# Kernel optimization log

Measured on AMD Instinct MI355X. Metric: run time of the kernel, lower is better.

Reference implementation:

```python
import jax, jax.numpy as jnp
import numpy as np

N = 1 << 20          # query points
RES = 160            # ceil((xyz_max - xyz_min)/voxel_size) = ceil(1/0.00625)
C = 12               # feature_dim
W = 128              # MLP width
NF = 2               # n_frame_features
FREQS = np.asarray([1.0, 2.0, 4.0, 8.0], np.float32)  # 2**linspace(0,3,4)
DIM0 = C + (3 + 2 * 3 * len(FREQS)) + NF              # 12 + 27 + 2 = 41
XYZ_MIN = np.zeros(3, np.float32)
XYZ_MAX = np.ones(3, np.float32)


def _lin_init(key, fan_in, fan_out):
    kw, kb = jax.random.split(key)
    s = 1.0 / np.sqrt(fan_in)
    w = jax.random.uniform(kw, (fan_in, fan_out), jnp.float32, -s, s)
    b = jax.random.uniform(kb, (fan_out,), jnp.float32, -s, s)
    return w, b


def setup_inputs() -> dict:
    key = jax.random.key(0)
    ks = jax.random.split(key, 10)
    pts = jax.random.uniform(ks[0], (N, 3), jnp.float32)          # inside [xyz_min, xyz_max]
    ff = jax.random.normal(ks[1], (N, NF), jnp.float32)           # frame features
    vd = jax.random.normal(ks[2], (N, 3), jnp.float32)            # view dirs
    vd = vd / jnp.linalg.norm(vd, axis=-1, keepdims=True)
    x = jnp.concatenate([pts, ff, vd], axis=-1)                   # [N, 8]
    grid = jax.random.normal(ks[3], (RES, RES, RES, C), jnp.float32) * 0.1
    dW1, db1 = _lin_init(ks[4], C, W)
    dW2, db2 = _lin_init(ks[5], W, W)
    dW3, _ = _lin_init(ks[6], W, 1)
    db3 = jnp.zeros((1,), jnp.float32)                            # constant bias init 0
    rW1, rb1 = _lin_init(ks[7], DIM0, W)
    rW2, rb2 = _lin_init(ks[8], W, W)
    rW3, _ = _lin_init(ks[9], W, 3)
    rb3 = jnp.zeros((3,), jnp.float32)
    return {"x": x, "grid": grid,
            "dW1": dW1, "db1": db1, "dW2": dW2, "db2": db2, "dW3": dW3, "db3": db3,
            "rW1": rW1, "rb1": rb1, "rW2": rW2, "rb2": rb2, "rW3": rW3, "rb3": rb3}


def trilinear(grid, pts):
    # DenseGrid: grid_sample(mode='bilinear', align_corners=True) on [C, Nx, Ny, Nz]
    R = grid.shape[0]
    u = jnp.clip((pts - XYZ_MIN) / (XYZ_MAX - XYZ_MIN), 0.0, 1.0)  # [N,3] in [0,1]
    pos = u * (R - 1)
    i0 = jnp.clip(jnp.floor(pos), 0, R - 2).astype(jnp.int32)      # [N,3]
    w = pos - i0.astype(pos.dtype)                                 # [N,3]
    g = grid.reshape(-1, grid.shape[-1])                           # [R^3, C]
    x0, y0, z0 = i0[:, 0], i0[:, 1], i0[:, 2]
    x1, y1, z1 = x0 + 1, y0 + 1, z0 + 1
    wx, wy, wz = w[:, 0:1], w[:, 1:2], w[:, 2:3]

    def gat(ix, iy, iz):
        return g[(ix * R + iy) * R + iz]                           # [N, C]

    return ((gat(x0, y0, z0) * (1 - wz) + gat(x0, y0, z1) * wz) * (1 - wy) +
            (gat(x0, y1, z0) * (1 - wz) + gat(x0, y1, z1) * wz) * wy) * (1 - wx) + \
           ((gat(x1, y0, z0) * (1 - wz) + gat(x1, y0, z1) * wz) * (1 - wy) +
            (gat(x1, y1, z0) * (1 - wz) + gat(x1, y1, z1) * wz) * wy) * wx


def view_embed(v):
    # include_input + sin/cos at freqs 2^[0..3]
    parts = [v]
    for f in FREQS:
        parts.append(jnp.sin(v * f))
        parts.append(jnp.cos(v * f))
    return jnp.concatenate(parts, axis=-1)  # [N, 27]


def reference(x, grid, dW1, db1, dW2, db2, dW3, db3, rW1, rb1, rW2, rb2, rW3, rb3):
    pts, ff, vd = x[:, :3], x[:, 3:3 + NF], x[:, 3 + NF:]
    feature = trilinear(grid, pts)                                  # [N, 12]
    h = jax.nn.relu(feature @ dW1 + db1)
    h = jax.nn.relu(h @ dW2 + db2)
    sdf = h @ dW3 + db3                                             # [N, 1]
    rgb_feat = jnp.concatenate([feature, view_embed(vd), ff], -1)  # [N, 41]
    h = jax.nn.relu(rgb_feat @ rW1 + rb1)
    h = jax.nn.relu(h @ rW2 + rb2)
    rgb = h @ rW3 + rb3                                             # [N, 3]
    return jnp.concatenate([rgb, sdf], -1)                          # [N, 4]
```

## Files before the change

### kernel.cpp

```cpp
#include <hip/hip_runtime.h>


#define NPTS   (1 << 20)
#define NCHUNK (NPTS / 64)

typedef _Float16 half8  __attribute__((ext_vector_type(8)));
typedef _Float16 half4_t __attribute__((ext_vector_type(4)));
typedef float    f32x4  __attribute__((ext_vector_type(4)));

#define OFF_DW1T 0
#define OFF_DW2T 4096
#define OFF_RW1A 20480
#define OFF_RW1B 24576
#define OFF_RW2T 28672
#define HALFS_TOTAL 45056
#define OFF_RW3T_BYTES (HALFS_TOTAL * 2)

#define HSTR 136
#define FSTR 40

__global__ void prep_weights(const float* __restrict__ dW1,
                             const float* __restrict__ dW2,
                             const float* __restrict__ rW1,
                             const float* __restrict__ rW2,
                             const float* __restrict__ rW3,
                             _Float16* __restrict__ wsh,
                             float* __restrict__ rw3t)
{
    int tid = blockIdx.x * 256 + threadIdx.x;
    if (tid >= 16384) return;
    int n = tid >> 7, k = tid & 127;
    wsh[OFF_DW2T + n*128 + k] = (_Float16)dW2[k*128 + n];
    wsh[OFF_RW2T + n*128 + k] = (_Float16)rW2[k*128 + n];
    if (k < 32) {
        wsh[OFF_DW1T + n*32 + k] = (k < 12) ? (_Float16)dW1[k*128 + n] : (_Float16)0.f;
        wsh[OFF_RW1A + n*32 + k] = (k < 12) ? (_Float16)rW1[k*128 + n] : (_Float16)0.f;
        wsh[OFF_RW1B + n*32 + k] = (k < 29) ? (_Float16)rW1[(12 + k)*128 + n] : (_Float16)0.f;
    }
    if (k < 3) rw3t[k*128 + n] = rW3[n*3 + k];
}

__device__ __forceinline__ void store_act(_Float16* buf, int n, int ub,
                                          f32x4 acc, const float* __restrict__ bias)
{
    float4 b4 = *(const float4*)(bias + ub);
    half4_t v;
    v[0] = (_Float16)fmaxf(acc[0] + b4.x, 0.f);
    v[1] = (_Float16)fmaxf(acc[1] + b4.y, 0.f);
    v[2] = (_Float16)fmaxf(acc[2] + b4.z, 0.f);
    v[3] = (_Float16)fmaxf(acc[3] + b4.w, 0.f);
    *(half4_t*)(buf + n*HSTR + ub) = v;
}

#define MFMA(a, b, c) __builtin_amdgcn_mfma_f32_16x16x32_f16((a), (b), (c), 0, 0, 0)

__global__ __launch_bounds__(256) void fastsurf_main(
    const float* __restrict__ x, const float* __restrict__ grid,
    const float* __restrict__ db1, const float* __restrict__ db2,
    const float* __restrict__ dW3, const float* __restrict__ db3,
    const float* __restrict__ rb1, const float* __restrict__ rb2,
    const float* __restrict__ rb3,
    const _Float16* __restrict__ wsh, const float* __restrict__ rw3t,
    float* __restrict__ out)
{
    __shared__ _Float16 featA[64 * FSTR];
    __shared__ _Float16 embA [64 * FSTR];
    __shared__ _Float16 h1buf[64 * HSTR];
    __shared__ _Float16 h2buf[64 * HSTR];

    const int t  = threadIdx.x;
    const int wv = t >> 6;
    const int l  = t & 63;
    const int ln = l & 15;
    const int qd = l >> 4;
    const int p  = t >> 2;
    const int q  = t & 3;
    const int u0 = (wv*2 + 0) * 16;
    const int u1 = (wv*2 + 1) * 16;

    half8 a_d2[2][4], a_r2[2][4];
#pragma unroll
    for (int rt = 0; rt < 2; ++rt) {
        const int m = (wv*2 + rt)*16 + ln;
#pragma unroll
        for (int ks = 0; ks < 4; ++ks) {
            a_d2[rt][ks] = *(const half8*)(wsh + OFF_DW2T + m*128 + ks*32 + qd*8);
            a_r2[rt][ks] = *(const half8*)(wsh + OFF_RW2T + m*128 + ks*32 + qd*8);
        }
    }

    for (int chunk = blockIdx.x; chunk < NCHUNK; chunk += gridDim.x) {
        const int pbase = chunk * 64;

        {
            const int P = pbase + p;
            const float4 xa = *(const float4*)(x + (size_t)P*8);
            const float4 xb = *(const float4*)(x + (size_t)P*8 + 4);
            float ux = fminf(fmaxf(xa.x, 0.f), 1.f) * 159.f;
            float uy = fminf(fmaxf(xa.y, 0.f), 1.f) * 159.f;
            float uz = fminf(fmaxf(xa.z, 0.f), 1.f) * 159.f;
            float fx = fminf(floorf(ux), 158.f);
            float fy = fminf(floorf(uy), 158.f);
            float fz = fminf(floorf(uz), 158.f);
            int ix = (int)fx, iy = (int)fy, iz = (int)fz;
            float wx = ux - fx, wy = uy - fy, wz = uz - fz;

            const int bx = q >> 1, by = q & 1;
            float wxy = (bx ? wx : 1.f - wx) * (by ? wy : 1.f - wy);
            float s0 = wxy * (1.f - wz), s1 = wxy * wz;
            const float* c = grid + (size_t)(((ix + bx)*160 + (iy + by))*160 + iz) * 12;
            float4 A0 = *(const float4*)(c);
            float4 A1 = *(const float4*)(c + 4);
            float4 A2 = *(const float4*)(c + 8);
            float4 B0 = *(const float4*)(c + 12);
            float4 B1 = *(const float4*)(c + 16);
            float4 B2 = *(const float4*)(c + 20);
            float f[12];
            f[0] = s0*A0.x + s1*B0.x;  f[1] = s0*A0.y + s1*B0.y;
            f[2] = s0*A0.z + s1*B0.z;  f[3] = s0*A0.w + s1*B0.w;
            f[4] = s0*A1.x + s1*B1.x;  f[5] = s0*A1.y + s1*B1.y;
            f[6] = s0*A1.z + s1*B1.z;  f[7] = s0*A1.w + s1*B1.w;
            f[8] = s0*A2.x + s1*B2.x;  f[9] = s0*A2.y + s1*B2.y;
            f[10]= s0*A2.z + s1*B2.z;  f[11]= s0*A2.w + s1*B2.w;
#pragma unroll
            for (int j = 0; j < 12; ++j) {
                f[j] += __shfl_xor(f[j], 1);
                f[j] += __shfl_xor(f[j], 2);
            }
            half8 fv = { (_Float16)0.f,(_Float16)0.f,(_Float16)0.f,(_Float16)0.f,
                         (_Float16)0.f,(_Float16)0.f,(_Float16)0.f,(_Float16)0.f };
            if (q == 0) {
                fv[0]=(_Float16)f[0]; fv[1]=(_Float16)f[1]; fv[2]=(_Float16)f[2]; fv[3]=(_Float16)f[3];
                fv[4]=(_Float16)f[4]; fv[5]=(_Float16)f[5]; fv[6]=(_Float16)f[6]; fv[7]=(_Float16)f[7];
            } else if (q == 1) {
                fv[0]=(_Float16)f[8]; fv[1]=(_Float16)f[9]; fv[2]=(_Float16)f[10]; fv[3]=(_Float16)f[11];
            }
            *(half8*)(featA + p*FSTR + q*8) = fv;

            const float v0 = xb.y, v1 = xb.z, v2 = xb.w;
            const float ff0 = xa.w, ff1 = xb.x;
            half8 ev = { (_Float16)0.f,(_Float16)0.f,(_Float16)0.f,(_Float16)0.f,
                         (_Float16)0.f,(_Float16)0.f,(_Float16)0.f,(_Float16)0.f };
            if (q == 0) {
                ev[0]=(_Float16)v0; ev[1]=(_Float16)v1; ev[2]=(_Float16)v2;
                ev[3]=(_Float16)__sinf(v0); ev[4]=(_Float16)__sinf(v1); ev[5]=(_Float16)__sinf(v2);
                ev[6]=(_Float16)__cosf(v0); ev[7]=(_Float16)__cosf(v1);
            } else if (q == 1) {
                ev[0]=(_Float16)__cosf(v2);
                ev[1]=(_Float16)__sinf(2.f*v0); ev[2]=(_Float16)__sinf(2.f*v1); ev[3]=(_Float16)__sinf(2.f*v2);
                ev[4]=(_Float16)__cosf(2.f*v0); ev[5]=(_Float16)__cosf(2.f*v1); ev[6]=(_Float16)__cosf(2.f*v2);
                ev[7]=(_Float16)__sinf(4.f*v0);
            } else if (q == 2) {
                ev[0]=(_Float16)__sinf(4.f*v1); ev[1]=(_Float16)__sinf(4.f*v2);
                ev[2]=(_Float16)__cosf(4.f*v0); ev[3]=(_Float16)__cosf(4.f*v1); ev[4]=(_Float16)__cosf(4.f*v2);
                ev[5]=(_Float16)__sinf(8.f*v0); ev[6]=(_Float16)__sinf(8.f*v1); ev[7]=(_Float16)__sinf(8.f*v2);
            } else {
                ev[0]=(_Float16)__cosf(8.f*v0); ev[1]=(_Float16)__cosf(8.f*v1); ev[2]=(_Float16)__cosf(8.f*v2);
                ev[3]=(_Float16)ff0; ev[4]=(_Float16)ff1;
            }
            *(half8*)(embA + p*FSTR + q*8) = ev;
        }
        __syncthreads();

        {
            const half8 a0 = *(const half8*)(wsh + OFF_DW1T + (u0 + ln)*32 + qd*8);
            const half8 a1 = *(const half8*)(wsh + OFF_DW1T + (u1 + ln)*32 + qd*8);
#pragma unroll
            for (int tl = 0; tl < 4; ++tl) {
                const int n = tl*16 + ln;
                half8 b = *(const half8*)(featA + n*FSTR + qd*8);
                f32x4 z = {0.f, 0.f, 0.f, 0.f};
                f32x4 acc0 = MFMA(a0, b, z);
                f32x4 acc1 = MFMA(a1, b, z);
                store_act(h1buf, n, u0 + qd*4, acc0, db1);
                store_act(h1buf, n, u1 + qd*4, acc1, db1);
            }
        }
        __syncthreads();

        {
#pragma unroll
            for (int tl = 0; tl < 4; ++tl) {
                const int n = tl*16 + ln;
                f32x4 acc0 = {0.f,0.f,0.f,0.f}, acc1 = {0.f,0.f,0.f,0.f};
#pragma unroll
                for (int ks = 0; ks < 4; ++ks) {
                    half8 b = *(const half8*)(h1buf + n*HSTR + ks*32 + qd*8);
                    acc0 = MFMA(a_d2[0][ks], b, acc0);
                    acc1 = MFMA(a_d2[1][ks], b, acc1);
                }
                store_act(h2buf, n, u0 + qd*4, acc0, db2);
                store_act(h2buf, n, u1 + qd*4, acc1, db2);
            }
        }
        __syncthreads();

        float sdf;
        {
            float s = 0.f;
#pragma unroll
            for (int i = 0; i < 4; ++i) {
                const int kb = q*32 + i*8;
                half8 hv = *(const half8*)(h2buf + p*HSTR + kb);
                float4 wa = *(const float4*)(dW3 + kb);
                float4 wb = *(const float4*)(dW3 + kb + 4);
                s += (float)hv[0]*wa.x + (float)hv[1]*wa.y + (float)hv[2]*wa.z + (float)hv[3]*wa.w
                   + (float)hv[4]*wb.x + (float)hv[5]*wb.y + (float)hv[6]*wb.z + (float)hv[7]*wb.w;
            }
            s += __shfl_xor(s, 1);
            s += __shfl_xor(s, 2);
            sdf = s + db3[0];
        }

        {
            const half8 aa0 = *(const half8*)(wsh + OFF_RW1A + (u0 + ln)*32 + qd*8);
            const half8 aa1 = *(const half8*)(wsh + OFF_RW1A + (u1 + ln)*32 + qd*8);
            const half8 ab0 = *(const half8*)(wsh + OFF_RW1B + (u0 + ln)*32 + qd*8);
            const half8 ab1 = *(const half8*)(wsh + OFF_RW1B + (u1 + ln)*32 + qd*8);
#pragma unroll
            for (int tl = 0; tl < 4; ++tl) {
                const int n = tl*16 + ln;
                half8 bf = *(const half8*)(featA + n*FSTR + qd*8);
                half8 be = *(const half8*)(embA  + n*FSTR + qd*8);
                f32x4 acc0 = {0.f,0.f,0.f,0.f}, acc1 = {0.f,0.f,0.f,0.f};
                acc0 = MFMA(aa0, bf, acc0);  acc0 = MFMA(ab0, be, acc0);
                acc1 = MFMA(aa1, bf, acc1);  acc1 = MFMA(ab1, be, acc1);
                store_act(h1buf, n, u0 + qd*4, acc0, rb1);
                store_act(h1buf, n, u1 + qd*4, acc1, rb1);
            }
        }
        __syncthreads();

        {
#pragma unroll
            for (int tl = 0; tl < 4; ++tl) {
                const int n = tl*16 + ln;
                f32x4 acc0 = {0.f,0.f,0.f,0.f}, acc1 = {0.f,0.f,0.f,0.f};
#pragma unroll
                for (int ks = 0; ks < 4; ++ks) {
                    half8 b = *(const half8*)(h1buf + n*HSTR + ks*32 + qd*8);
                    acc0 = MFMA(a_r2[0][ks], b, acc0);
                    acc1 = MFMA(a_r2[1][ks], b, acc1);
                }
                store_act(h2buf, n, u0 + qd*4, acc0, rb2);
                store_act(h2buf, n, u1 + qd*4, acc1, rb2);
            }
        }
        __syncthreads();

        {
            float r0 = 0.f, r1 = 0.f, r2 = 0.f;
#pragma unroll
            for (int i = 0; i < 4; ++i) {
                const int kb = q*32 + i*8;
                half8 hv = *(const half8*)(h2buf + p*HSTR + kb);
                float h0=hv[0], h1v=hv[1], h2v=hv[2], h3=hv[3], h4=hv[4], h5=hv[5], h6=hv[6], h7=hv[7];
                {
                    float4 wa = *(const float4*)(rw3t + kb);
                    float4 wb = *(const float4*)(rw3t + kb + 4);
                    r0 += h0*wa.x + h1v*wa.y + h2v*wa.z + h3*wa.w + h4*wb.x + h5*wb.y + h6*wb.z + h7*wb.w;
                }
                {
                    float4 wa = *(const float4*)(rw3t + 128 + kb);
                    float4 wb = *(const float4*)(rw3t + 128 + kb + 4);
                    r1 += h0*wa.x + h1v*wa.y + h2v*wa.z + h3*wa.w + h4*wb.x + h5*wb.y + h6*wb.z + h7*wb.w;
                }
                {
                    float4 wa = *(const float4*)(rw3t + 256 + kb);
                    float4 wb = *(const float4*)(rw3t + 256 + kb + 4);
                    r2 += h0*wa.x + h1v*wa.y + h2v*wa.z + h3*wa.w + h4*wb.x + h5*wb.y + h6*wb.z + h7*wb.w;
                }
            }
            r0 += __shfl_xor(r0, 1);  r0 += __shfl_xor(r0, 2);
            r1 += __shfl_xor(r1, 1);  r1 += __shfl_xor(r1, 2);
            r2 += __shfl_xor(r2, 1);  r2 += __shfl_xor(r2, 2);
            if (q == 0) {
                float4 o;
                o.x = r0 + rb3[0];
                o.y = r1 + rb3[1];
                o.z = r2 + rb3[2];
                o.w = sdf;
                *(float4*)(out + (size_t)(pbase + p)*4) = o;
            }
        }
        __syncthreads();
    }
}

extern "C" void kernel_launch(void* const* d_in, const int* in_sizes, int n_in,
                              void* d_out, int out_size, void* d_ws, size_t ws_size,
                              hipStream_t stream) {
    const float* x    = (const float*)d_in[0];
    const float* grid = (const float*)d_in[1];
    const float* dW1  = (const float*)d_in[2];
    const float* db1  = (const float*)d_in[3];
    const float* dW2  = (const float*)d_in[4];
    const float* db2  = (const float*)d_in[5];
    const float* dW3  = (const float*)d_in[6];
    const float* db3  = (const float*)d_in[7];
    const float* rW1  = (const float*)d_in[8];
    const float* rb1  = (const float*)d_in[9];
    const float* rW2  = (const float*)d_in[10];
    const float* rb2  = (const float*)d_in[11];
    const float* rW3  = (const float*)d_in[12];
    const float* rb3  = (const float*)d_in[13];
    float* out = (float*)d_out;

    _Float16* wsh = (_Float16*)d_ws;
    float* rw3t = (float*)((char*)d_ws + OFF_RW3T_BYTES);

    prep_weights<<<64, 256, 0, stream>>>(dW1, dW2, rW1, rW2, rW3, wsh, rw3t);
    fastsurf_main<<<1024, 256, 0, stream>>>(x, grid, db1, db2, dW3, db3,
                                            rb1, rb2, rb3, wsh, rw3t, out);
}
```

Measured before the change: 668.2 us.

## Prefetch next chunk's gathers and merge density/RGB MLP stages to cut barriers

The input points and trilinear corner gathers for the next chunk are software-prefetched into registers while the current chunk's MLPs run. A barrier that waits only on LDS counters lets those global loads stay in flight across synchronisation points. The density and RGB MLP layers are merged stage by stage into separate LDS buffers, which cuts the per-chunk barriers from six to three. The cost is roughly double the shared memory plus extra prefetch registers, which may reduce occupancy.

Measured after the change: 767.0 us. 14.8% more time.

```diff
diff --git a/kernel.cpp b/kernel.cpp
--- a/kernel.cpp
+++ b/kernel.cpp
@@ -54,6 +54,29 @@
 
 #define MFMA(a, b, c) __builtin_amdgcn_mfma_f32_16x16x32_f16((a), (b), (c), 0, 0, 0)
 
+__device__ __forceinline__ void wg_barrier() {
+    asm volatile("s_waitcnt lgkmcnt(0)" ::: "memory");
+    __builtin_amdgcn_s_barrier();
+}
+
+__device__ __forceinline__ const float* corner_addr(const float* __restrict__ grid,
+                                                    float4 xa, int bx, int by,
+                                                    float& s0, float& s1)
+{
+    float ux = fminf(fmaxf(xa.x, 0.f), 1.f) * 159.f;
+    float uy = fminf(fmaxf(xa.y, 0.f), 1.f) * 159.f;
+    float uz = fminf(fmaxf(xa.z, 0.f), 1.f) * 159.f;
+    float fx = fminf(floorf(ux), 158.f);
+    float fy = fminf(floorf(uy), 158.f);
+    float fz = fminf(floorf(uz), 158.f);
+    int ix = (int)fx, iy = (int)fy, iz = (int)fz;
+    float wx = ux - fx, wy = uy - fy, wz = uz - fz;
+    float wxy = (bx ? wx : 1.f - wx) * (by ? wy : 1.f - wy);
+    s0 = wxy * (1.f - wz);
+    s1 = wxy * wz;
+    return grid + (size_t)(((ix + bx)*160 + (iy + by))*160 + iz) * 12;
+}
+
 __global__ __launch_bounds__(256) void fastsurf_main(
     const float* __restrict__ x, const float* __restrict__ grid,
     const float* __restrict__ db1, const float* __restrict__ db2,
@@ -67,6 +90,8 @@
     __shared__ _Float16 embA [64 * FSTR];
     __shared__ _Float16 h1buf[64 * HSTR];
     __shared__ _Float16 h2buf[64 * HSTR];
+    __shared__ _Float16 g1buf[64 * HSTR];
+    __shared__ _Float16 g2buf[64 * HSTR];
 
     const int t  = threadIdx.x;
     const int wv = t >> 6;
@@ -75,8 +100,10 @@
     const int qd = l >> 4;
     const int p  = t >> 2;
     const int q  = t & 3;
+    const int bx = q >> 1, by = q & 1;
     const int u0 = (wv*2 + 0) * 16;
     const int u1 = (wv*2 + 1) * 16;
+    const int STEP = gridDim.x;
 
     half8 a_d2[2][4], a_r2[2][4];
 #pragma unroll
@@ -89,39 +116,37 @@
         }
     }
 
-    for (int chunk = blockIdx.x; chunk < NCHUNK; chunk += gridDim.x) {
+    float4 xc_a, xc_b;
+    float4 xn_a, xn_b;
+    float  s0c, s1c;
+    float4 gA0, gA1, gA2, gB0, gB1, gB2;
+
+    {
+        int c0 = blockIdx.x;
+        int c1 = c0 + STEP; if (c1 >= NCHUNK) c1 = c0;
+        size_t P0 = (size_t)c0*64 + p;
+        xc_a = *(const float4*)(x + P0*8);
+        xc_b = *(const float4*)(x + P0*8 + 4);
+        size_t P1 = (size_t)c1*64 + p;
+        xn_a = *(const float4*)(x + P1*8);
+        xn_b = *(const float4*)(x + P1*8 + 4);
+        const float* cb = corner_addr(grid, xc_a, bx, by, s0c, s1c);
+        gA0 = *(const float4*)(cb);      gA1 = *(const float4*)(cb + 4);
+        gA2 = *(const float4*)(cb + 8);  gB0 = *(const float4*)(cb + 12);
+        gB1 = *(const float4*)(cb + 16); gB2 = *(const float4*)(cb + 20);
+    }
+
+    for (int chunk = blockIdx.x; chunk < NCHUNK; chunk += STEP) {
         const int pbase = chunk * 64;
 
         {
-            const int P = pbase + p;
-            const float4 xa = *(const float4*)(x + (size_t)P*8);
-            const float4 xb = *(const float4*)(x + (size_t)P*8 + 4);
-            float ux = fminf(fmaxf(xa.x, 0.f), 1.f) * 159.f;
-            float uy = fminf(fmaxf(xa.y, 0.f), 1.f) * 159.f;
-            float uz = fminf(fmaxf(xa.z, 0.f), 1.f) * 159.f;
-            float fx = fminf(floorf(ux), 158.f);
-            float fy = fminf(floorf(uy), 158.f);
-            float fz = fminf(floorf(uz), 158.f);
-            int ix = (int)fx, iy = (int)fy, iz = (int)fz;
-            float wx = ux - fx, wy = uy - fy, wz = uz - fz;
-
-            const int bx = q >> 1, by = q & 1;
-            float wxy = (bx ? wx : 1.f - wx) * (by ? wy : 1.f - wy);
-            float s0 = wxy * (1.f - wz), s1 = wxy * wz;
-            const float* c = grid + (size_t)(((ix + bx)*160 + (iy + by))*160 + iz) * 12;
-            float4 A0 = *(const float4*)(c);
-            float4 A1 = *(const float4*)(c + 4);
-            float4 A2 = *(const float4*)(c + 8);
-            float4 B0 = *(const float4*)(c + 12);
-            float4 B1 = *(const float4*)(c + 16);
-            float4 B2 = *(const float4*)(c + 20);
             float f[12];
-            f[0] = s0*A0.x + s1*B0.x;  f[1] = s0*A0.y + s1*B0.y;
-            f[2] = s0*A0.z + s1*B0.z;  f[3] = s0*A0.w + s1*B0.w;
-            f[4] = s0*A1.x + s1*B1.x;  f[5] = s0*A1.y + s1*B1.y;
-            f[6] = s0*A1.z + s1*B1.z;  f[7] = s0*A1.w + s1*B1.w;
-            f[8] = s0*A2.x + s1*B2.x;  f[9] = s0*A2.y + s1*B2.y;
-            f[10]= s0*A2.z + s1*B2.z;  f[11]= s0*A2.w + s1*B2.w;
+            f[0] = s0c*gA0.x + s1c*gB0.x;  f[1] = s0c*gA0.y + s1c*gB0.y;
+            f[2] = s0c*gA0.z + s1c*gB0.z;  f[3] = s0c*gA0.w + s1c*gB0.w;
+            f[4] = s0c*gA1.x + s1c*gB1.x;  f[5] = s0c*gA1.y + s1c*gB1.y;
+            f[6] = s0c*gA1.z + s1c*gB1.z;  f[7] = s0c*gA1.w + s1c*gB1.w;
+            f[8] = s0c*gA2.x + s1c*gB2.x;  f[9] = s0c*gA2.y + s1c*gB2.y;
+            f[10]= s0c*gA2.z + s1c*gB2.z;  f[11]= s0c*gA2.w + s1c*gB2.w;
 #pragma unroll
             for (int j = 0; j < 12; ++j) {
                 f[j] += __shfl_xor(f[j], 1);
@@ -137,8 +162,8 @@
             }
             *(half8*)(featA + p*FSTR + q*8) = fv;
 
-            const float v0 = xb.y, v1 = xb.z, v2 = xb.w;
-            const float ff0 = xa.w, ff1 = xb.x;
+            const float v0 = xc_b.y, v1 = xc_b.z, v2 = xc_b.w;
+            const float ff0 = xc_a.w, ff1 = xc_b.x;
             half8 ev = { (_Float16)0.f,(_Float16)0.f,(_Float16)0.f,(_Float16)0.f,
                          (_Float16)0.f,(_Float16)0.f,(_Float16)0.f,(_Float16)0.f };
             if (q == 0) {
@@ -160,23 +185,46 @@
             }
             *(half8*)(embA + p*FSTR + q*8) = ev;
         }
-        __syncthreads();
-
-        {
-            const half8 a0 = *(const half8*)(wsh + OFF_DW1T + (u0 + ln)*32 + qd*8);
-            const half8 a1 = *(const half8*)(wsh + OFF_DW1T + (u1 + ln)*32 + qd*8);
+
+        {
+            float s0n, s1n;
+            const float* cb = corner_addr(grid, xn_a, bx, by, s0n, s1n);
+            xc_a = xn_a; xc_b = xn_b;
+            s0c = s0n;  s1c = s1n;
+            gA0 = *(const float4*)(cb);      gA1 = *(const float4*)(cb + 4);
+            gA2 = *(const float4*)(cb + 8);  gB0 = *(const float4*)(cb + 12);
+            gB1 = *(const float4*)(cb + 16); gB2 = *(const float4*)(cb + 20);
+            int c2 = chunk + 2*STEP; if (c2 >= NCHUNK) c2 = chunk;
+            size_t P2 = (size_t)c2*64 + p;
+            xn_a = *(const float4*)(x + P2*8);
+            xn_b = *(const float4*)(x + P2*8 + 4);
+        }
+        wg_barrier();
+
+        {
+            const half8 ad0 = *(const half8*)(wsh + OFF_DW1T + (u0 + ln)*32 + qd*8);
+            const half8 ad1 = *(const half8*)(wsh + OFF_DW1T + (u1 + ln)*32 + qd*8);
+            const half8 aa0 = *(const half8*)(wsh + OFF_RW1A + (u0 + ln)*32 + qd*8);
+            const half8 aa1 = *(const half8*)(wsh + OFF_RW1A + (u1 + ln)*32 + qd*8);
+            const half8 ab0 = *(const half8*)(wsh + OFF_RW1B + (u0 + ln)*32 + qd*8);
+            const half8 ab1 = *(const half8*)(wsh + OFF_RW1B + (u1 + ln)*32 + qd*8);
 #pragma unroll
             for (int tl = 0; tl < 4; ++tl) {
                 const int n = tl*16 + ln;
-                half8 b = *(const half8*)(featA + n*FSTR + qd*8);
+                half8 bf = *(const half8*)(featA + n*FSTR + qd*8);
+                half8 be = *(const half8*)(embA  + n*FSTR + qd*8);
                 f32x4 z = {0.f, 0.f, 0.f, 0.f};
-                f32x4 acc0 = MFMA(a0, b, z);
-                f32x4 acc1 = MFMA(a1, b, z);
-                store_act(h1buf, n, u0 + qd*4, acc0, db1);
-                store_act(h1buf, n, u1 + qd*4, acc1, db1);
-            }
-        }
-        __syncthreads();
+                f32x4 d0 = MFMA(ad0, bf, z);
+                f32x4 d1 = MFMA(ad1, bf, z);
+                store_act(h1buf, n, u0 + qd*4, d0, db1);
+                store_act(h1buf, n, u1 + qd*4, d1, db1);
+                f32x4 r0 = MFMA(aa0, bf, z);  r0 = MFMA(ab0, be, r0);
+                f32x4 r1 = MFMA(aa1, bf, z);  r1 = MFMA(ab1, be, r1);
+                store_act(g1buf, n, u0 + qd*4, r0, rb1);
+                store_act(g1buf, n, u1 + qd*4, r1, rb1);
+            }
+        }
+        wg_barrier();
 
         {
 #pragma unroll
@@ -191,70 +239,33 @@
                 }
                 store_act(h2buf, n, u0 + qd*4, acc0, db2);
                 store_act(h2buf, n, u1 + qd*4, acc1, db2);
-            }
-        }
-        __syncthreads();
-
-        float sdf;
-        {
-            float s = 0.f;
+                f32x4 rcc0 = {0.f,0.f,0.f,0.f}, rcc1 = {0.f,0.f,0.f,0.f};
+#pragma unroll
+                for (int ks = 0; ks < 4; ++ks) {
+                    half8 b = *(const half8*)(g1buf + n*HSTR + ks*32 + qd*8);
+                    rcc0 = MFMA(a_r2[0][ks], b, rcc0);
+                    rcc1 = MFMA(a_r2[1][ks], b, rcc1);
+                }
+                store_act(g2buf, n, u0 + qd*4, rcc0, rb2);
+                store_act(g2buf, n, u1 + qd*4, rcc1, rb2);
+            }
+        }
+        wg_barrier();
+
+        {
+            float sacc = 0.f, r0 = 0.f, r1 = 0.f, r2 = 0.f;
 #pragma unroll
             for (int i = 0; i < 4; ++i) {
                 const int kb = q*32 + i*8;
                 half8 hv = *(const half8*)(h2buf + p*HSTR + kb);
-                float4 wa = *(const float4*)(dW3 + kb);
-                float4 wb = *(const float4*)(dW3 + kb + 4);
-                s += (float)hv[0]*wa.x + (float)hv[1]*wa.y + (float)hv[2]*wa.z + (float)hv[3]*wa.w
-                   + (float)hv[4]*wb.x + (float)hv[5]*wb.y + (float)hv[6]*wb.z + (float)hv[7]*wb.w;
-            }
-            s += __shfl_xor(s, 1);
-            s += __shfl_xor(s, 2);
-            sdf = s + db3[0];
-        }
-
-        {
-            const half8 aa0 = *(const half8*)(wsh + OFF_RW1A + (u0 + ln)*32 + qd*8);
-            const half8 aa1 = *(const half8*)(wsh + OFF_RW1A + (u1 + ln)*32 + qd*8);
-            const half8 ab0 = *(const half8*)(wsh + OFF_RW1B + (u0 + ln)*32 + qd*8);
-            const half8 ab1 = *(const half8*)(wsh + OFF_RW1B + (u1 + ln)*32 + qd*8);
-#pragma unroll
-            for (int tl = 0; tl < 4; ++tl) {
-                const int n = tl*16 + ln;
-                half8 bf = *(const half8*)(featA + n*FSTR + qd*8);
-                half8 be = *(const half8*)(embA  + n*FSTR + qd*8);
-                f32x4 acc0 = {0.f,0.f,0.f,0.f}, acc1 = {0.f,0.f,0.f,0.f};
-                acc0 = MFMA(aa0, bf, acc0);  acc0 = MFMA(ab0, be, acc0);
-                acc1 = MFMA(aa1, bf, acc1);  acc1 = MFMA(ab1, be, acc1);
-                store_act(h1buf, n, u0 + qd*4, acc0, rb1);
-                store_act(h1buf, n, u1 + qd*4, acc1, rb1);
-            }
-        }
-        __syncthreads();
-
-        {
-#pragma unroll
-            for (int tl = 0; tl < 4; ++tl) {
-                const int n = tl*16 + ln;
-                f32x4 acc0 = {0.f,0.f,0.f,0.f}, acc1 = {0.f,0.f,0.f,0.f};
-#pragma unroll
-                for (int ks = 0; ks < 4; ++ks) {
-                    half8 b = *(const half8*)(h1buf + n*HSTR + ks*32 + qd*8);
-                    acc0 = MFMA(a_r2[0][ks], b, acc0);
-                    acc1 = MFMA(a_r2[1][ks], b, acc1);
-                }
-                store_act(h2buf, n, u0 + qd*4, acc0, rb2);
-                store_act(h2buf, n, u1 + qd*4, acc1, rb2);
-            }
-        }
-        __syncthreads();
-
-        {
-            float r0 = 0.f, r1 = 0.f, r2 = 0.f;
-#pragma unroll
-            for (int i = 0; i < 4; ++i) {
-                const int kb = q*32 + i*8;
-                half8 hv = *(const half8*)(h2buf + p*HSTR + kb);
-                float h0=hv[0], h1v=hv[1], h2v=hv[2], h3=hv[3], h4=hv[4], h5=hv[5], h6=hv[6], h7=hv[7];
+                {
+                    float4 wa = *(const float4*)(dW3 + kb);
+                    float4 wb = *(const float4*)(dW3 + kb + 4);
+                    sacc += (float)hv[0]*wa.x + (float)hv[1]*wa.y + (float)hv[2]*wa.z + (float)hv[3]*wa.w
+                          + (float)hv[4]*wb.x + (float)hv[5]*wb.y + (float)hv[6]*wb.z + (float)hv[7]*wb.w;
+                }
+                half8 gv = *(const half8*)(g2buf + p*HSTR + kb);
+                float h0=gv[0], h1v=gv[1], h2v=gv[2], h3=gv[3], h4=gv[4], h5=gv[5], h6=gv[6], h7=gv[7];
                 {
                     float4 wa = *(const float4*)(rw3t + kb);
                     float4 wb = *(const float4*)(rw3t + kb + 4);
@@ -271,6 +282,7 @@
                     r2 += h0*wa.x + h1v*wa.y + h2v*wa.z + h3*wa.w + h4*wb.x + h5*wb.y + h6*wb.z + h7*wb.w;
                 }
             }
+            sacc += __shfl_xor(sacc, 1);  sacc += __shfl_xor(sacc, 2);
             r0 += __shfl_xor(r0, 1);  r0 += __shfl_xor(r0, 2);
             r1 += __shfl_xor(r1, 1);  r1 += __shfl_xor(r1, 2);
             r2 += __shfl_xor(r2, 1);  r2 += __shfl_xor(r2, 2);
@@ -279,11 +291,10 @@
                 o.x = r0 + rb3[0];
                 o.y = r1 + rb3[1];
                 o.z = r2 + rb3[2];
-                o.w = sdf;
+                o.w = sacc + db3[0];
                 *(float4*)(out + (size_t)(pbase + p)*4) = o;
             }
         }
-        __syncthreads();
     }
 }
 
```

## Swizzle LDS activations, run output layers on MFMA, reload layer-2 weights per chunk

Applied to the files above, without the earlier changes.

Replaces the padded LDS strides with an XOR-swizzled layout for the feature/embedding and hidden buffers, merging the feature and embedding buffers into one. The final sdf and rgb projections now use MFMA with fp16 weights prepared in workspace, replacing the scalar dot products and shuffle reductions. Layer-2 weight fragments are loaded from global/L2 inside each chunk instead of being held in registers across the loop, and launch bounds request 4 blocks per CU. This cuts register pressure and LDS bank conflicts, at the cost of repeated weight loads and fp16 rounding of the output weights.

Result: slower. 784.4 us (+17.4%).

```diff
diff --git a/kernel.cpp b/kernel.cpp
--- a/kernel.cpp
+++ b/kernel.cpp
@@ -4,28 +4,26 @@
 #define NPTS   (1 << 20)
 #define NCHUNK (NPTS / 64)
 
-typedef _Float16 half8  __attribute__((ext_vector_type(8)));
+typedef _Float16 half8   __attribute__((ext_vector_type(8)));
 typedef _Float16 half4_t __attribute__((ext_vector_type(4)));
-typedef float    f32x4  __attribute__((ext_vector_type(4)));
+typedef float    f32x4   __attribute__((ext_vector_type(4)));
 
 #define OFF_DW1T 0
 #define OFF_DW2T 4096
 #define OFF_RW1A 20480
 #define OFF_RW1B 24576
 #define OFF_RW2T 28672
-#define HALFS_TOTAL 45056
-#define OFF_RW3T_BYTES (HALFS_TOTAL * 2)
-
-#define HSTR 136
-#define FSTR 40
+#define OFF_RGBA 45056
+#define OFF_SDFA 45568
+#define HALFS_TOTAL 45696
 
 __global__ void prep_weights(const float* __restrict__ dW1,
                              const float* __restrict__ dW2,
+                             const float* __restrict__ dW3,
                              const float* __restrict__ rW1,
                              const float* __restrict__ rW2,
                              const float* __restrict__ rW3,
-                             _Float16* __restrict__ wsh,
-                             float* __restrict__ rw3t)
+                             _Float16* __restrict__ wsh)
 {
     int tid = blockIdx.x * 256 + threadIdx.x;
     if (tid >= 16384) return;
@@ -37,7 +35,8 @@
         wsh[OFF_RW1A + n*32 + k] = (k < 12) ? (_Float16)rW1[k*128 + n] : (_Float16)0.f;
         wsh[OFF_RW1B + n*32 + k] = (k < 29) ? (_Float16)rW1[(12 + k)*128 + n] : (_Float16)0.f;
     }
-    if (k < 3) rw3t[k*128 + n] = rW3[n*3 + k];
+    if (n < 4)  wsh[OFF_RGBA + n*128 + k] = (n < 3) ? (_Float16)rW3[k*3 + n] : (_Float16)0.f;
+    if (n == 0) wsh[OFF_SDFA + k] = (_Float16)dW3[k];
 }
 
 __device__ __forceinline__ void store_act(_Float16* buf, int n, int ub,
@@ -49,24 +48,27 @@
     v[1] = (_Float16)fmaxf(acc[1] + b4.y, 0.f);
     v[2] = (_Float16)fmaxf(acc[2] + b4.z, 0.f);
     v[3] = (_Float16)fmaxf(acc[3] + b4.w, 0.f);
-    *(half4_t*)(buf + n*HSTR + ub) = v;
+    const int u = ub >> 3;
+    *(half4_t*)(buf + n*128 + ((u ^ (n & 7)) << 3) + (ub & 7)) = v;
 }
 
 #define MFMA(a, b, c) __builtin_amdgcn_mfma_f32_16x16x32_f16((a), (b), (c), 0, 0, 0)
 
-__global__ __launch_bounds__(256) void fastsurf_main(
+#define HRD(buf, n, ks, qd) (*(const half8*)((buf) + (n)*128 + ((((ks)*4 + (qd)) ^ ((n) & 7)) << 3)))
+#define FRD(n, u) (*(const half8*)(fe + (n)*64 + (((u) ^ ((n) & 7)) << 3)))
+
+__global__ __launch_bounds__(256, 4) void fastsurf_main(
     const float* __restrict__ x, const float* __restrict__ grid,
     const float* __restrict__ db1, const float* __restrict__ db2,
-    const float* __restrict__ dW3, const float* __restrict__ db3,
+    const float* __restrict__ db3,
     const float* __restrict__ rb1, const float* __restrict__ rb2,
     const float* __restrict__ rb3,
-    const _Float16* __restrict__ wsh, const float* __restrict__ rw3t,
+    const _Float16* __restrict__ wsh,
     float* __restrict__ out)
 {
-    __shared__ _Float16 featA[64 * FSTR];
-    __shared__ _Float16 embA [64 * FSTR];
-    __shared__ _Float16 h1buf[64 * HSTR];
-    __shared__ _Float16 h2buf[64 * HSTR];
+    __shared__ _Float16 fe[64 * 64];
+    __shared__ _Float16 h1[64 * 128];
+    __shared__ _Float16 h2[64 * 128];
 
     const int t  = threadIdx.x;
     const int wv = t >> 6;
@@ -78,16 +80,8 @@
     const int u0 = (wv*2 + 0) * 16;
     const int u1 = (wv*2 + 1) * 16;
 
-    half8 a_d2[2][4], a_r2[2][4];
-#pragma unroll
-    for (int rt = 0; rt < 2; ++rt) {
-        const int m = (wv*2 + rt)*16 + ln;
-#pragma unroll
-        for (int ks = 0; ks < 4; ++ks) {
-            a_d2[rt][ks] = *(const half8*)(wsh + OFF_DW2T + m*128 + ks*32 + qd*8);
-            a_r2[rt][ks] = *(const half8*)(wsh + OFF_RW2T + m*128 + ks*32 + qd*8);
-        }
-    }
+    const float db3v = db3[0];
+    const float rb30 = rb3[0], rb31 = rb3[1], rb32 = rb3[2];
 
     for (int chunk = blockIdx.x; chunk < NCHUNK; chunk += gridDim.x) {
         const int pbase = chunk * 64;
@@ -135,7 +129,7 @@
             } else if (q == 1) {
                 fv[0]=(_Float16)f[8]; fv[1]=(_Float16)f[9]; fv[2]=(_Float16)f[10]; fv[3]=(_Float16)f[11];
             }
-            *(half8*)(featA + p*FSTR + q*8) = fv;
+            *(half8*)(fe + p*64 + ((q ^ (p & 7)) << 3)) = fv;
 
             const float v0 = xb.y, v1 = xb.z, v2 = xb.w;
             const float ff0 = xa.w, ff1 = xb.x;
@@ -158,7 +152,7 @@
                 ev[0]=(_Float16)__cosf(8.f*v0); ev[1]=(_Float16)__cosf(8.f*v1); ev[2]=(_Float16)__cosf(8.f*v2);
                 ev[3]=(_Float16)ff0; ev[4]=(_Float16)ff1;
             }
-            *(half8*)(embA + p*FSTR + q*8) = ev;
+            *(half8*)(fe + p*64 + (((4 + q) ^ (p & 7)) << 3)) = ev;
         }
         __syncthreads();
 
@@ -168,48 +162,48 @@
 #pragma unroll
             for (int tl = 0; tl < 4; ++tl) {
                 const int n = tl*16 + ln;
-                half8 b = *(const half8*)(featA + n*FSTR + qd*8);
+                half8 b = FRD(n, qd);
                 f32x4 z = {0.f, 0.f, 0.f, 0.f};
                 f32x4 acc0 = MFMA(a0, b, z);
                 f32x4 acc1 = MFMA(a1, b, z);
-                store_act(h1buf, n, u0 + qd*4, acc0, db1);
-                store_act(h1buf, n, u1 + qd*4, acc1, db1);
-            }
-        }
-        __syncthreads();
-
-        {
+                store_act(h1, n, u0 + qd*4, acc0, db1);
+                store_act(h1, n, u1 + qd*4, acc1, db1);
+            }
+        }
+        __syncthreads();
+
+        {
+            half8 a_d[2][4];
+#pragma unroll
+            for (int rt = 0; rt < 2; ++rt)
+#pragma unroll
+                for (int ks = 0; ks < 4; ++ks)
+                    a_d[rt][ks] = *(const half8*)(wsh + OFF_DW2T + ((wv*2 + rt)*16 + ln)*128 + ks*32 + qd*8);
 #pragma unroll
             for (int tl = 0; tl < 4; ++tl) {
                 const int n = tl*16 + ln;
                 f32x4 acc0 = {0.f,0.f,0.f,0.f}, acc1 = {0.f,0.f,0.f,0.f};
 #pragma unroll
                 for (int ks = 0; ks < 4; ++ks) {
-                    half8 b = *(const half8*)(h1buf + n*HSTR + ks*32 + qd*8);
-                    acc0 = MFMA(a_d2[0][ks], b, acc0);
-                    acc1 = MFMA(a_d2[1][ks], b, acc1);
+                    half8 b = HRD(h1, n, ks, qd);
+                    acc0 = MFMA(a_d[0][ks], b, acc0);
+                    acc1 = MFMA(a_d[1][ks], b, acc1);
                 }
-                store_act(h2buf, n, u0 + qd*4, acc0, db2);
-                store_act(h2buf, n, u1 + qd*4, acc1, db2);
-            }
-        }
-        __syncthreads();
-
-        float sdf;
-        {
-            float s = 0.f;
-#pragma unroll
-            for (int i = 0; i < 4; ++i) {
-                const int kb = q*32 + i*8;
-                half8 hv = *(const half8*)(h2buf + p*HSTR + kb);
-                float4 wa = *(const float4*)(dW3 + kb);
-                float4 wb = *(const float4*)(dW3 + kb + 4);
-                s += (float)hv[0]*wa.x + (float)hv[1]*wa.y + (float)hv[2]*wa.z + (float)hv[3]*wa.w
-                   + (float)hv[4]*wb.x + (float)hv[5]*wb.y + (float)hv[6]*wb.z + (float)hv[7]*wb.w;
-            }
-            s += __shfl_xor(s, 1);
-            s += __shfl_xor(s, 2);
-            sdf = s + db3[0];
+                store_act(h2, n, u0 + qd*4, acc0, db2);
+                store_act(h2, n, u1 + qd*4, acc1, db2);
+            }
+        }
+        __syncthreads();
+
+        f32x4 sacc = {0.f, 0.f, 0.f, 0.f};
+        {
+            const int n = wv*16 + ln;
+#pragma unroll
+            for (int ks = 0; ks < 4; ++ks) {
+                half8 a = *(const half8*)(wsh + OFF_SDFA + ks*32 + qd*8);
+                half8 b = HRD(h2, n, ks, qd);
+                sacc = MFMA(a, b, sacc);
+            }
         }
 
         {
@@ -220,67 +214,56 @@
 #pragma unroll
             for (int tl = 0; tl < 4; ++tl) {
                 const int n = tl*16 + ln;
-                half8 bf = *(const half8*)(featA + n*FSTR + qd*8);
-                half8 be = *(const half8*)(embA  + n*FSTR + qd*8);
+                half8 bf = FRD(n, qd);
+                half8 be = FRD(n, 4 + qd);
+                f32x4 z = {0.f, 0.f, 0.f, 0.f};
+                f32x4 acc0 = MFMA(aa0, bf, z);  acc0 = MFMA(ab0, be, acc0);
+                f32x4 acc1 = MFMA(aa1, bf, z);  acc1 = MFMA(ab1, be, acc1);
+                store_act(h1, n, u0 + qd*4, acc0, rb1);
+                store_act(h1, n, u1 + qd*4, acc1, rb1);
+            }
+        }
+        __syncthreads();
+
+        {
+            half8 a_r[2][4];
+#pragma unroll
+            for (int rt = 0; rt < 2; ++rt)
+#pragma unroll
+                for (int ks = 0; ks < 4; ++ks)
+                    a_r[rt][ks] = *(const half8*)(wsh + OFF_RW2T + ((wv*2 + rt)*16 + ln)*128 + ks*32 + qd*8);
+#pragma unroll
+            for (int tl = 0; tl < 4; ++tl) {
+                const int n = tl*16 + ln;
                 f32x4 acc0 = {0.f,0.f,0.f,0.f}, acc1 = {0.f,0.f,0.f,0.f};
-                acc0 = MFMA(aa0, bf, acc0);  acc0 = MFMA(ab0, be, acc0);
-                acc1 = MFMA(aa1, bf, acc1);  acc1 = MFMA(ab1, be, acc1);
-                store_act(h1buf, n, u0 + qd*4, acc0, rb1);
-                store_act(h1buf, n, u1 + qd*4, acc1, rb1);
-            }
-        }
-        __syncthreads();
-
-        {
-#pragma unroll
-            for (int tl = 0; tl < 4; ++tl) {
-                const int n = tl*16 + ln;
-                f32x4 acc0 = {0.f,0.f,0.f,0.f}, acc1 = {0.f,0.f,0.f,0.f};
 #pragma unroll
                 for (int ks = 0; ks < 4; ++ks) {
-                    half8 b = *(const half8*)(h1buf + n*HSTR + ks*32 + qd*8);
-                    acc0 = MFMA(a_r2[0][ks], b, acc0);
-                    acc1 = MFMA(a_r2[1][ks], b, acc1);
+                    half8 b = HRD(h1, n, ks, qd);
+                    acc0 = MFMA(a_r[0][ks], b, acc0);
+                    acc1 = MFMA(a_r[1][ks], b, acc1);
                 }
-                store_act(h2buf, n, u0 + qd*4, acc0, rb2);
-                store_act(h2buf, n, u1 + qd*4, acc1, rb2);
-            }
-        }
-        __syncthreads();
-
-        {
-            float r0 = 0.f, r1 = 0.f, r2 = 0.f;
-#pragma unroll
-            for (int i = 0; i < 4; ++i) {
-                const int kb = q*32 + i*8;
-                half8 hv = *(const half8*)(h2buf + p*HSTR + kb);
-                float h0=hv[0], h1v=hv[1], h2v=hv[2], h3=hv[3], h4=hv[4], h5=hv[5], h6=hv[6], h7=hv[7];
-                {
-                    float4 wa = *(const float4*)(rw3t + kb);
-                    float4 wb = *(const float4*)(rw3t + kb + 4);
-                    r0 += h0*wa.x + h1v*wa.y + h2v*wa.z + h3*wa.w + h4*wb.x + h5*wb.y + h6*wb.z + h7*wb.w;
-                }
-                {
-                    float4 wa = *(const float4*)(rw3t + 128 + kb);
-                    float4 wb = *(const float4*)(rw3t + 128 + kb + 4);
-                    r1 += h0*wa.x + h1v*wa.y + h2v*wa.z + h3*wa.w + h4*wb.x + h5*wb.y + h6*wb.z + h7*wb.w;
-                }
-                {
-                    float4 wa = *(const float4*)(rw3t + 256 + kb);
-                    float4 wb = *(const float4*)(rw3t + 256 + kb + 4);
-                    r2 += h0*wa.x + h1v*wa.y + h2v*wa.z + h3*wa.w + h4*wb.x + h5*wb.y + h6*wb.z + h7*wb.w;
-                }
-            }
-            r0 += __shfl_xor(r0, 1);  r0 += __shfl_xor(r0, 2);
-            r1 += __shfl_xor(r1, 1);  r1 += __shfl_xor(r1, 2);
-            r2 += __shfl_xor(r2, 1);  r2 += __shfl_xor(r2, 2);
-            if (q == 0) {
+                store_act(h2, n, u0 + qd*4, acc0, rb2);
+                store_act(h2, n, u1 + qd*4, acc1, rb2);
+            }
+        }
+        __syncthreads();
+
+        {
+            f32x4 racc = {0.f, 0.f, 0.f, 0.f};
+            const int n = wv*16 + ln;
+#pragma unroll
+            for (int ks = 0; ks < 4; ++ks) {
+                half8 a = *(const half8*)(wsh + OFF_RGBA + (ln & 3)*128 + ks*32 + qd*8);
+                half8 b = HRD(h2, n, ks, qd);
+                racc = MFMA(a, b, racc);
+            }
+            if (qd == 0) {
                 float4 o;
-                o.x = r0 + rb3[0];
-                o.y = r1 + rb3[1];
-                o.z = r2 + rb3[2];
-                o.w = sdf;
-                *(float4*)(out + (size_t)(pbase + p)*4) = o;
+                o.x = racc[0] + rb30;
+                o.y = racc[1] + rb31;
+                o.z = racc[2] + rb32;
+                o.w = sacc[0] + db3v;
+                *(float4*)(out + (size_t)(pbase + n)*4) = o;
             }
         }
         __syncthreads();
@@ -307,9 +290,8 @@
     float* out = (float*)d_out;
 
     _Float16* wsh = (_Float16*)d_ws;
-    float* rw3t = (float*)((char*)d_ws + OFF_RW3T_BYTES);
-
-    prep_weights<<<64, 256, 0, stream>>>(dW1, dW2, rW1, rW2, rW3, wsh, rw3t);
-    fastsurf_main<<<1024, 256, 0, stream>>>(x, grid, db1, db2, dW3, db3,
-                                            rb1, rb2, rb3, wsh, rw3t, out);
-}
+
+    prep_weights<<<64, 256, 0, stream>>>(dW1, dW2, dW3, rW1, rW2, rW3, wsh);
+    fastsurf_main<<<1024, 256, 0, stream>>>(x, grid, db1, db2, db3,
+                                            rb1, rb2, rb3, wsh, out);
+}
```
